# Performance work log

Hardware: AMD Instinct MI355X
Metric: run time of the kernel (lower is better)

## Reference

```python
import jax, jax.numpy as jnp
from jax import lax
import numpy as np

FEAT_SIZES = [38, 19, 10, 5, 3, 1]
IN_CH = [512, 1024, 512, 256, 256, 256]
NUM_ANCH = [4, 6, 6, 6, 4, 4]
NUM_CLASSES = 91
BATCH = 32


def _conv3x3(x, w, b):
    # x: [N, C, H, W], w: [O, C, 3, 3] (OIHW), padding=1, stride=1
    y = lax.conv_general_dilated(x, w, window_strides=(1, 1), padding=((1, 1), (1, 1)),
                                 dimension_numbers=("NCHW", "OIHW", "NCHW"))
    return y + b[None, :, None, None]


def _scoring_head(feats, ws, bs, num_cols):
    # Faithful to SSDScoringHead.forward: per-level conv, reshape
    # (N, A*num_cols, H, W) -> (N, H*W*A, num_cols), concat over levels.
    outs = []
    for x, w, b in zip(feats, ws, bs):
        r = _conv3x3(x, w, b)
        N, _, H, W = r.shape
        r = r.reshape(N, -1, num_cols, H, W)          # [N, A, C, H, W]
        r = jnp.transpose(r, (0, 3, 4, 1, 2))          # [N, H, W, A, C]
        r = r.reshape(N, -1, num_cols)                 # [N, H*W*A, C]
        outs.append(r)
    return jnp.concatenate(outs, axis=1)


def setup_inputs() -> dict:
    key = jax.random.key(0)
    inp = {}
    k = key
    for i, (c, s, a) in enumerate(zip(IN_CH, FEAT_SIZES, NUM_ANCH)):
        k, k1, k2, k3 = jax.random.split(k, 4)
        inp[f"feat{i}"] = jax.random.normal(k1, (BATCH, c, s, s), dtype=jnp.float32)
        fan = c * 9
        scale = (2.0 / fan) ** 0.5
        inp[f"cls_w{i}"] = jax.random.normal(k2, (NUM_CLASSES * a, c, 3, 3), dtype=jnp.float32) * scale
        inp[f"cls_b{i}"] = jnp.zeros((NUM_CLASSES * a,), dtype=jnp.float32)
        inp[f"reg_w{i}"] = jax.random.normal(k3, (4 * a, c, 3, 3), dtype=jnp.float32) * scale
        inp[f"reg_b{i}"] = jnp.zeros((4 * a,), dtype=jnp.float32)
    return inp


def reference(feat0, feat1, feat2, feat3, feat4, feat5,
              cls_w0, cls_b0, reg_w0, reg_b0,
              cls_w1, cls_b1, reg_w1, reg_b1,
              cls_w2, cls_b2, reg_w2, reg_b2,
              cls_w3, cls_b3, reg_w3, reg_b3,
              cls_w4, cls_b4, reg_w4, reg_b4,
              cls_w5, cls_b5, reg_w5, reg_b5):
    feats = [feat0, feat1, feat2, feat3, feat4, feat5]
    cls_ws = [cls_w0, cls_w1, cls_w2, cls_w3, cls_w4, cls_w5]
    cls_bs = [cls_b0, cls_b1, cls_b2, cls_b3, cls_b4, cls_b5]
    reg_ws = [reg_w0, reg_w1, reg_w2, reg_w3, reg_w4, reg_w5]
    reg_bs = [reg_b0, reg_b1, reg_b2, reg_b3, reg_b4, reg_b5]
    bbox_regression = _scoring_head(feats, reg_ws, reg_bs, 4)          # [N, 8732, 4]
    cls_logits = _scoring_head(feats, cls_ws, cls_bs, NUM_CLASSES)     # [N, 8732, 91]
    return (bbox_regression, cls_logits)
```

## Files before the change

kernel.cpp:

```cpp
#include <hip/hip_runtime.h>

typedef __attribute__((ext_vector_type(8))) short short8;
typedef __attribute__((ext_vector_type(4))) short short4x;
typedef __attribute__((ext_vector_type(4))) float floatx4;

#define DEVI __device__ __forceinline__

#define GLL(g, l) __builtin_amdgcn_global_load_lds(                      \
    (const __attribute__((address_space(1))) void*)(g),                  \
    (__attribute__((address_space(3))) void*)(l), 16, 0, 0)

constexpr int LC[6]   = {512, 1024, 512, 256, 256, 256};
constexpr int LS[6]   = {38, 19, 10, 5, 3, 1};
constexpr int LA[6]   = {4, 6, 6, 6, 4, 4};
constexpr int LROW[6] = {0, 5776, 7942, 8542, 8692, 8728};
constexpr long FOFF[6] = {0, 23658496, 35487744, 37126144, 37330944, 37404672};
constexpr long WCBASE  = 37412864;
constexpr long WOFF[6] = {0, 1751040, 7004160, 9630720, 10944000, 11819520};
constexpr long ZOFF    = 50107904;
constexpr int  ZSIZE   = 1088;
constexpr long CLSOFF  = 1117696;
constexpr size_t WS_NEEDED = (size_t)(ZOFF + ZSIZE) * 2;

constexpr int RSTART[7] = {0, 380, 950, 1520, 2090, 2470, 2850};
constexpr int GB_T5 = 0, GB_T4 = 8, GB_T3 = 16, GB_T2 = 40, GB_T1 = 112, GB_T0 = 344, GB_TOT = 888;

DEVI short f2bf(float f) {
    union { float f; unsigned u; } x; x.f = f;
    unsigned u = x.u + 0x7fffu + ((x.u >> 16) & 1u);
    return (short)(u >> 16);
}

template<int L>
__global__ void transpose_feat(const float* __restrict__ feat, short* __restrict__ ft) {
    constexpr int C = LC[L], S = LS[L], HW = S * S;
    const int n  = blockIdx.z;
    const int p0 = blockIdx.x * 64;
    const int c0 = blockIdx.y * 64;
    __shared__ float tile[64][65];
    const int t = threadIdx.x;
    const float* fb = feat + ((size_t)n * C + c0) * HW;
#pragma unroll
    for (int e = 0; e < 16; ++e) {
        int idx = e * 256 + t;
        int p = idx & 63, cc = idx >> 6;
        int pix = p0 + p;
        tile[cc][p] = (pix < HW) ? fb[(size_t)cc * HW + pix] : 0.f;
    }
    __syncthreads();
    short* ob = ft + ((size_t)n * HW) * C + c0;
#pragma unroll
    for (int e = 0; e < 16; ++e) {
        int idx = e * 256 + t;
        int cc = idx & 63, p = idx >> 6;
        int pix = p0 + p;
        if (pix < HW) ob[(size_t)pix * C + cc] = f2bf(tile[cc][p]);
    }
}

struct WPtrs { const float* cw[6]; const float* rw[6]; };

template<int L>
DEVI void reorder_body(int o, const float* cw, const float* rw, short* wc, short* wlds) {
    constexpr int C = LC[L], K9 = 9 * C, A4 = 4 * LA[L];
    constexpr int LC2 = (C == 1024) ? 10 : (C == 512 ? 9 : 8);
    const int tid = threadIdx.x;
    const float* src = (o < A4) ? rw + (size_t)o * K9 : cw + (size_t)(o - A4) * K9;
#pragma unroll 1
    for (int i4 = tid; i4 < K9 / 4; i4 += 256) {
        floatx4 v = *(const floatx4*)(src + 4 * i4);
        short4x s;
#pragma unroll
        for (int j = 0; j < 4; ++j) s[j] = f2bf(v[j]);
        *(short4x*)(wlds + 4 * i4) = s;
    }
    __syncthreads();
    short* dst = wc + WOFF[L] + (size_t)o * K9;
#pragma unroll 1
    for (int g = tid; g < K9 / 8; g += 256) {
        const int k0 = g * 8;
        const int r  = k0 >> LC2;
        const int c0 = k0 & (C - 1);
        short8 v;
#pragma unroll
        for (int j = 0; j < 8; ++j) v[j] = wlds[(c0 + j) * 9 + r];
        *(short8*)(dst + k0) = v;
    }
}

__global__ __launch_bounds__(256)
void reorder_weights2(WPtrs p, short* __restrict__ wc, short* __restrict__ zb) {
    __shared__ short wlds[9216];
    const int b = blockIdx.x;
    if (b >= RSTART[6]) {
        if (threadIdx.x < ZSIZE / 8) {
            short8 z;
#pragma unroll
            for (int q = 0; q < 8; ++q) z[q] = 0;
            *(short8*)(zb + threadIdx.x * 8) = z;
        }
        return;
    }
    if (b >= RSTART[5])      reorder_body<5>(b - RSTART[5], p.cw[5], p.rw[5], wc, wlds);
    else if (b >= RSTART[4]) reorder_body<4>(b - RSTART[4], p.cw[4], p.rw[4], wc, wlds);
    else if (b >= RSTART[3]) reorder_body<3>(b - RSTART[3], p.cw[3], p.rw[3], wc, wlds);
    else if (b >= RSTART[2]) reorder_body<2>(b - RSTART[2], p.cw[2], p.rw[2], wc, wlds);
    else if (b >= RSTART[1]) reorder_body<1>(b - RSTART[1], p.cw[1], p.rw[1], wc, wlds);
    else                     reorder_body<0>(b,             p.cw[0], p.rw[0], wc, wlds);
}

template<int L>
DEVI void gemm_body(int lb, short* As, short* Bs,
                    const short* ft, const short* wc, const short* zb,
                    const float* cls_b, const float* reg_b, float* out)
{
    constexpr int C = LC[L], S = LS[L], A = LA[L];
    constexpr int HW = S * S, M = 32 * HW, K = 9 * C, O = 95 * A;
    constexpr int ROWOFF = LROW[L], A4 = 4 * A;
    constexpr int NM = (M + 255) / 256, NB = (O + 127) / 128;
    constexpr int TOT = NM * NB, TPX = (TOT + 7) / 8;
    constexpr int KC  = C / 32;
    constexpr int LKC = (C == 1024) ? 5 : (C == 512 ? 4 : 3);
    constexpr int NK  = 9 * KC;

    const int tt = (lb & 7) * TPX + (lb >> 3);
    if (tt >= TOT) return;
    const int m0 = (tt / NB) * 256;
    const int n0 = (tt % NB) * 128;

    const int t    = threadIdx.x;
    const int lane = t & 63;
    const int wid  = t >> 6;
    const int lrow = lane >> 2;
    const int kqe  = (lane & 3) ^ ((lane >> 3) & 3);

    const short* abase[4]; unsigned vmask[4];
#pragma unroll
    for (int j = 0; j < 4; ++j) {
        int m = m0 + wid * 64 + j * 16 + lrow;
        int mm = m < M ? m : (M - 1);
        int n = mm / HW;
        int rem = mm - n * HW;
        int y = rem / S, x = rem - (rem / S) * S;
        abase[j] = ft + ((size_t)n * HW + rem) * C + kqe * 8;
        unsigned msk = 0;
#pragma unroll
        for (int r = 0; r < 9; ++r) {
            int dy = r / 3 - 1, dx = r % 3 - 1;
            if ((unsigned)(y + dy) < (unsigned)S && (unsigned)(x + dx) < (unsigned)S)
                msk |= 1u << r;
        }
        vmask[j] = msk;
    }
    const short* bbase[2];
#pragma unroll
    for (int j = 0; j < 2; ++j) {
        int o = n0 + wid * 32 + j * 16 + lrow;
        if (o >= O) o = O - 1;
        bbase[j] = wc + (size_t)o * K + kqe * 8;
    }
    const short* zbl = zb + kqe * 8;

    const int wm    = (wid & 1) * 128;
    const int wn    = (wid >> 1) * 64;
    const int lcol  = lane & 15;
    const int lquad = lane >> 4;
    const int rq8   = (lquad ^ ((lcol >> 1) & 3)) * 8;

    floatx4 acc[8][4];
#pragma unroll
    for (int i = 0; i < 8; ++i)
#pragma unroll
        for (int j = 0; j < 4; ++j)
#pragma unroll
            for (int q = 0; q < 4; ++q) acc[i][j][q] = 0.f;

    auto stage = [&](int kk, int p) {
        const int r  = kk >> LKC;
        const int c0 = (kk & (KC - 1)) << 5;
        const int dy = r / 3 - 1, dx = r - (r / 3) * 3 - 1;
        const int roA = (dy * S + dx) * C + c0;
        const int roB = r * C + c0;
        short* ap = As + p * 8192;
        short* bp = Bs + p * 4096;
#pragma unroll
        for (int j = 0; j < 4; ++j) {
            const short* pa = ((vmask[j] >> r) & 1) ? abase[j] + roA : zbl + c0;
            GLL(pa, ap + (wid * 64 + j * 16) * 32);
        }
        GLL(bbase[0] + roB, bp + (wid * 32) * 32);
        GLL(bbase[1] + roB, bp + (wid * 32 + 16) * 32);
    };
    auto frags = [&](int p, short8* af, short8* bfr) {
        const short* ap = As + p * 8192;
        const short* bp = Bs + p * 4096;
#pragma unroll
        for (int f = 0; f < 8; ++f)
            af[f] = *(const short8*)&ap[(wm + f * 16 + lcol) * 32 + rq8];
#pragma unroll
        for (int f = 0; f < 4; ++f)
            bfr[f] = *(const short8*)&bp[(wn + f * 16 + lcol) * 32 + rq8];
    };
    auto mmac = [&](short8* af, short8* bfr) {
#pragma unroll
        for (int i = 0; i < 8; ++i)
#pragma unroll
            for (int j = 0; j < 4; ++j)
                acc[i][j] = __builtin_amdgcn_mfma_f32_16x16x32_bf16(af[i], bfr[j], acc[i][j], 0, 0, 0);
    };

    stage(0, 0);
    stage(1, 1);
    asm volatile("s_waitcnt vmcnt(6)" ::: "memory");
    __builtin_amdgcn_s_barrier();
    int p = 0, pn = 2;
#pragma unroll 1
    for (int kk = 0; kk < NK - 2; ++kk) {
        short8 af[8], bfr[4];
        frags(p, af, bfr);
        stage(kk + 2, pn);
        asm volatile("s_waitcnt vmcnt(6)" ::: "memory");
        __builtin_amdgcn_s_barrier();
        asm volatile("s_waitcnt lgkmcnt(0)" ::: "memory");
        __builtin_amdgcn_s_setprio(1);
        mmac(af, bfr);
        __builtin_amdgcn_s_setprio(0);
        __builtin_amdgcn_s_barrier();
        p  = (p  == 2) ? 0 : p  + 1;
        pn = (pn == 2) ? 0 : pn + 1;
    }
    {
        short8 af[8], bfr[4];
        frags((NK - 2) % 3, af, bfr);
        asm volatile("s_waitcnt vmcnt(0)" ::: "memory");
        __builtin_amdgcn_s_barrier();
        asm volatile("s_waitcnt lgkmcnt(0)" ::: "memory");
        __builtin_amdgcn_s_setprio(1);
        mmac(af, bfr);
        __builtin_amdgcn_s_setprio(0);
    }
    {
        short8 af[8], bfr[4];
        frags((NK - 1) % 3, af, bfr);
        mmac(af, bfr);
    }

    float* const bbox = out;
    float* const cls  = out + CLSOFF;
#pragma unroll
    for (int fn = 0; fn < 4; ++fn) {
        const int o = n0 + wn + fn * 16 + lcol;
        if (o < O) {
            if (o < A4) {
                const int aa = o >> 2, cc = o & 3;
                const float bias = reg_b[o];
#pragma unroll
                for (int fm = 0; fm < 8; ++fm)
#pragma unroll
                    for (int rg = 0; rg < 4; ++rg) {
                        int mr = m0 + wm + fm * 16 + lquad * 4 + rg;
                        if (mr < M) {
                            int n = mr / HW, rem = mr - n * HW;
                            bbox[((size_t)n * 8732 + ROWOFF + rem * A + aa) * 4 + cc] = acc[fm][fn][rg] + bias;
                        }
                    }
            } else {
                const int oc = o - A4;
                const int aa = oc / 91, cc = oc - aa * 91;
                const float bias = cls_b[oc];
#pragma unroll
                for (int fm = 0; fm < 8; ++fm)
#pragma unroll
                    for (int rg = 0; rg < 4; ++rg) {
                        int mr = m0 + wm + fm * 16 + lquad * 4 + rg;
                        if (mr < M) {
                            int n = mr / HW, rem = mr - n * HW;
                            cls[((size_t)n * 8732 + ROWOFF + rem * A + aa) * 91 + cc] = acc[fm][fn][rg] + bias;
                        }
                    }
            }
        }
    }
}

struct GArgs {
    const short* ft[6];
    const short* wcL[6];
    const short* zb;
    const float* cb[6];
    const float* rb[6];
    float* out;
};

__global__ __launch_bounds__(256, 2)
void gemm_all(GArgs a) {
    __shared__ __align__(16) short As[3 * 8192];
    __shared__ __align__(16) short Bs[3 * 4096];
    const int b = blockIdx.x;
    if (b >= GB_T0)      gemm_body<0>(b - GB_T0, As, Bs, a.ft[0], a.wcL[0], a.zb, a.cb[0], a.rb[0], a.out);
    else if (b >= GB_T1) gemm_body<1>(b - GB_T1, As, Bs, a.ft[1], a.wcL[1], a.zb, a.cb[1], a.rb[1], a.out);
    else if (b >= GB_T2) gemm_body<2>(b - GB_T2, As, Bs, a.ft[2], a.wcL[2], a.zb, a.cb[2], a.rb[2], a.out);
    else if (b >= GB_T3) gemm_body<3>(b - GB_T3, As, Bs, a.ft[3], a.wcL[3], a.zb, a.cb[3], a.rb[3], a.out);
    else if (b >= GB_T4) gemm_body<4>(b - GB_T4, As, Bs, a.ft[4], a.wcL[4], a.zb, a.cb[4], a.rb[4], a.out);
    else                 gemm_body<5>(b - GB_T5, As, Bs, a.ft[5], a.wcL[5], a.zb, a.cb[5], a.rb[5], a.out);
}

template<int L>
__global__ void naive_conv(const float* __restrict__ feat,
                           const float* __restrict__ cw, const float* __restrict__ cb,
                           const float* __restrict__ rw, const float* __restrict__ rb,
                           float* __restrict__ out)
{
    constexpr int C = LC[L], S = LS[L], A = LA[L];
    constexpr int HW = S * S, M = 32 * HW, A4 = 4 * A, ROWOFF = LROW[L];
    int m = blockIdx.x * 256 + threadIdx.x;
    if (m >= M) return;
    int o = blockIdx.y;
    int n = m / HW, rem = m - n * HW, h = rem / S, w = rem - (rem / S) * S;
    bool isreg = o < A4;
    const float* wr = isreg ? (rw + (size_t)o * C * 9) : (cw + (size_t)(o - A4) * C * 9);
    float sum = isreg ? rb[o] : cb[o - A4];
    const float* fb = feat + (size_t)n * C * HW;
    for (int c = 0; c < C; ++c) {
#pragma unroll
        for (int r = 0; r < 9; ++r) {
            int y = h + r / 3 - 1, x = w + r % 3 - 1;
            if ((unsigned)y < (unsigned)S && (unsigned)x < (unsigned)S)
                sum += wr[c * 9 + r] * fb[(size_t)c * HW + y * S + x];
        }
    }
    int rowidx = ROWOFF + rem * A;
    if (isreg) out[((size_t)n * 8732 + rowidx + (o >> 2)) * 4 + (o & 3)] = sum;
    else {
        int oc = o - A4;
        int a = oc / 91;
        (out + CLSOFF)[((size_t)n * 8732 + rowidx + a) * 91 + (oc - a * 91)] = sum;
    }
}

extern "C" void kernel_launch(void* const* d_in, const int* in_sizes, int n_in,
                              void* d_out, int out_size, void* d_ws, size_t ws_size,
                              hipStream_t stream)
{
    const float *feat[6], *cw[6], *cb[6], *rw[6], *rb[6];
    for (int i = 0; i < 6; ++i) {
        feat[i] = (const float*)d_in[5 * i + 0];
        cw[i]   = (const float*)d_in[5 * i + 1];
        cb[i]   = (const float*)d_in[5 * i + 2];
        rw[i]   = (const float*)d_in[5 * i + 3];
        rb[i]   = (const float*)d_in[5 * i + 4];
    }
    float* out = (float*)d_out;

    if (ws_size >= WS_NEEDED) {
        short* ws  = (short*)d_ws;
        short* wcp = ws + WCBASE;
        short* zb  = ws + ZOFF;
        transpose_feat<0><<<dim3(23, 8, 32), 256, 0, stream>>>(feat[0], ws + FOFF[0]);
        transpose_feat<1><<<dim3(6, 16, 32), 256, 0, stream>>>(feat[1], ws + FOFF[1]);
        transpose_feat<2><<<dim3(2, 8, 32), 256, 0, stream>>>(feat[2], ws + FOFF[2]);
        transpose_feat<3><<<dim3(1, 4, 32), 256, 0, stream>>>(feat[3], ws + FOFF[3]);
        transpose_feat<4><<<dim3(1, 4, 32), 256, 0, stream>>>(feat[4], ws + FOFF[4]);
        transpose_feat<5><<<dim3(1, 4, 32), 256, 0, stream>>>(feat[5], ws + FOFF[5]);
        WPtrs wp;
        for (int i = 0; i < 6; ++i) { wp.cw[i] = cw[i]; wp.rw[i] = rw[i]; }
        reorder_weights2<<<RSTART[6] + 1, 256, 0, stream>>>(wp, wcp, zb);
        GArgs ga;
        for (int i = 0; i < 6; ++i) {
            ga.ft[i]  = ws + FOFF[i];
            ga.wcL[i] = wcp + WOFF[i];
            ga.cb[i]  = cb[i];
            ga.rb[i]  = rb[i];
        }
        ga.zb  = zb;
        ga.out = out;
        gemm_all<<<GB_TOT, 256, 0, stream>>>(ga);
    } else {
        naive_conv<0><<<dim3(181, 380), 256, 0, stream>>>(feat[0], cw[0], cb[0], rw[0], rb[0], out);
        naive_conv<1><<<dim3(46, 570),  256, 0, stream>>>(feat[1], cw[1], cb[1], rw[1], rb[1], out);
        naive_conv<2><<<dim3(13, 570),  256, 0, stream>>>(feat[2], cw[2], cb[2], rw[2], rb[2], out);
        naive_conv<3><<<dim3(4, 570),   256, 0, stream>>>(feat[3], cw[3], cb[3], rw[3], rb[3], out);
        naive_conv<4><<<dim3(2, 380),   256, 0, stream>>>(feat[4], cw[4], cb[4], rw[4], rb[4], out);
        naive_conv<5><<<dim3(1, 380),   256, 0, stream>>>(feat[5], cw[5], cb[5], rw[5], rb[5], out);
    }
}
```

Baseline: 715.1 us.

## Merge prep kernels into one launch and restructure GEMM k-loop barrier pipeline

Folds the six feature transpose kernels, the weight reorder kernel and the zero-fill into a single prep_all launch that dispatches on block index over a shared LDS buffer, removing several launches and the tail gaps between them. The GEMM main loop now issues the next stage's global-to-LDS loads before reading fragments, uses a sched_barrier, and defers the vmcnt wait and barrier until after the MFMAs, leaving one barrier per iteration instead of two. This is meant to overlap LDS fragment reads and global loads with matrix math. With the triple buffer, the correctness of the single barrier depends on the buffer rotation keeping stage and read slots apart.

```diff
diff --git a/kernel.cpp b/kernel.cpp
--- a/kernel.cpp
+++ b/kernel.cpp
@@ -25,6 +25,13 @@
 constexpr int RSTART[7] = {0, 380, 950, 1520, 2090, 2470, 2850};
 constexpr int GB_T5 = 0, GB_T4 = 8, GB_T3 = 16, GB_T2 = 40, GB_T1 = 112, GB_T0 = 344, GB_TOT = 888;
 
+constexpr int PPX[6] = {23, 6, 2, 1, 1, 1};
+constexpr int PCY[6] = {8, 16, 8, 4, 4, 4};
+constexpr int PSTART[7] = {0, 5888, 8960, 9472, 9600, 9728, 9856};
+constexpr int PREORD = 9856;
+constexpr int PZERO  = PREORD + 2850;
+constexpr int PTOT   = PZERO + 1;
+
 DEVI short f2bf(float f) {
     union { float f; unsigned u; } x; x.f = f;
     unsigned u = x.u + 0x7fffu + ((x.u >> 16) & 1u);
@@ -32,12 +39,11 @@
 }
 
 template<int L>
-__global__ void transpose_feat(const float* __restrict__ feat, short* __restrict__ ft) {
+DEVI void transpose_body(int bx, int by, int n, const float* __restrict__ feat,
+                         short* __restrict__ ft, float (*tile)[65]) {
     constexpr int C = LC[L], S = LS[L], HW = S * S;
-    const int n  = blockIdx.z;
-    const int p0 = blockIdx.x * 64;
-    const int c0 = blockIdx.y * 64;
-    __shared__ float tile[64][65];
+    const int p0 = bx * 64;
+    const int c0 = by * 64;
     const int t = threadIdx.x;
     const float* fb = feat + ((size_t)n * C + c0) * HW;
 #pragma unroll
@@ -57,8 +63,6 @@
         if (pix < HW) ob[(size_t)pix * C + cc] = f2bf(tile[cc][p]);
     }
 }
-
-struct WPtrs { const float* cw[6]; const float* rw[6]; };
 
 template<int L>
 DEVI void reorder_body(int o, const float* cw, const float* rw, short* wc, short* wlds) {
@@ -88,25 +92,56 @@
     }
 }
 
+struct PrepArgs {
+    const float* feat[6];
+    const float* cw[6];
+    const float* rw[6];
+    short* ft[6];
+    short* wc;
+    short* zb;
+};
+
 __global__ __launch_bounds__(256)
-void reorder_weights2(WPtrs p, short* __restrict__ wc, short* __restrict__ zb) {
-    __shared__ short wlds[9216];
+void prep_all(PrepArgs a) {
+    __shared__ __align__(16) char PL[18432];
+    float (*tile)[65] = reinterpret_cast<float(*)[65]>(PL);
+    short* wlds = reinterpret_cast<short*>(PL);
     const int b = blockIdx.x;
-    if (b >= RSTART[6]) {
+    if (b >= PZERO) {
         if (threadIdx.x < ZSIZE / 8) {
             short8 z;
 #pragma unroll
             for (int q = 0; q < 8; ++q) z[q] = 0;
-            *(short8*)(zb + threadIdx.x * 8) = z;
+            *(short8*)(a.zb + threadIdx.x * 8) = z;
         }
         return;
     }
-    if (b >= RSTART[5])      reorder_body<5>(b - RSTART[5], p.cw[5], p.rw[5], wc, wlds);
-    else if (b >= RSTART[4]) reorder_body<4>(b - RSTART[4], p.cw[4], p.rw[4], wc, wlds);
-    else if (b >= RSTART[3]) reorder_body<3>(b - RSTART[3], p.cw[3], p.rw[3], wc, wlds);
-    else if (b >= RSTART[2]) reorder_body<2>(b - RSTART[2], p.cw[2], p.rw[2], wc, wlds);
-    else if (b >= RSTART[1]) reorder_body<1>(b - RSTART[1], p.cw[1], p.rw[1], wc, wlds);
-    else                     reorder_body<0>(b,             p.cw[0], p.rw[0], wc, wlds);
+    if (b >= PREORD) {
+        int rb = b - PREORD;
+        if (rb >= RSTART[5])      reorder_body<5>(rb - RSTART[5], a.cw[5], a.rw[5], a.wc, wlds);
+        else if (rb >= RSTART[4]) reorder_body<4>(rb - RSTART[4], a.cw[4], a.rw[4], a.wc, wlds);
+        else if (rb >= RSTART[3]) reorder_body<3>(rb - RSTART[3], a.cw[3], a.rw[3], a.wc, wlds);
+        else if (rb >= RSTART[2]) reorder_body<2>(rb - RSTART[2], a.cw[2], a.rw[2], a.wc, wlds);
+        else if (rb >= RSTART[1]) reorder_body<1>(rb - RSTART[1], a.cw[1], a.rw[1], a.wc, wlds);
+        else                      reorder_body<0>(rb,             a.cw[0], a.rw[0], a.wc, wlds);
+        return;
+    }
+#define TDISP(L)                                                              \
+    {                                                                         \
+        int r = b - PSTART[L];                                                \
+        int bx = r % PPX[L];                                                  \
+        int by = (r / PPX[L]) % PCY[L];                                       \
+        int n  = r / (PPX[L] * PCY[L]);                                       \
+        transpose_body<L>(bx, by, n, a.feat[L], a.ft[L], tile);               \
+        return;                                                               \
+    }
+    if (b >= PSTART[5])      TDISP(5)
+    else if (b >= PSTART[4]) TDISP(4)
+    else if (b >= PSTART[3]) TDISP(3)
+    else if (b >= PSTART[2]) TDISP(2)
+    else if (b >= PSTART[1]) TDISP(1)
+    else                     TDISP(0)
+#undef TDISP
 }
 
 template<int L>
@@ -217,31 +252,30 @@
 #pragma unroll 1
     for (int kk = 0; kk < NK - 2; ++kk) {
         short8 af[8], bfr[4];
+        stage(kk + 2, pn);
         frags(p, af, bfr);
-        stage(kk + 2, pn);
-        asm volatile("s_waitcnt vmcnt(6)" ::: "memory");
-        __builtin_amdgcn_s_barrier();
-        asm volatile("s_waitcnt lgkmcnt(0)" ::: "memory");
+        __builtin_amdgcn_sched_barrier(0);
         __builtin_amdgcn_s_setprio(1);
         mmac(af, bfr);
         __builtin_amdgcn_s_setprio(0);
+        asm volatile("s_waitcnt vmcnt(6)" ::: "memory");
         __builtin_amdgcn_s_barrier();
         p  = (p  == 2) ? 0 : p  + 1;
         pn = (pn == 2) ? 0 : pn + 1;
     }
     {
         short8 af[8], bfr[4];
-        frags((NK - 2) % 3, af, bfr);
-        asm volatile("s_waitcnt vmcnt(0)" ::: "memory");
-        __builtin_amdgcn_s_barrier();
-        asm volatile("s_waitcnt lgkmcnt(0)" ::: "memory");
+        frags(p, af, bfr);
         __builtin_amdgcn_s_setprio(1);
         mmac(af, bfr);
         __builtin_amdgcn_s_setprio(0);
+        asm volatile("s_waitcnt vmcnt(0)" ::: "memory");
+        __builtin_amdgcn_s_barrier();
+        p = (p == 2) ? 0 : p + 1;
     }
     {
         short8 af[8], bfr[4];
-        frags((NK - 1) % 3, af, bfr);
+        frags(p, af, bfr);
         mmac(af, bfr);
     }
 
@@ -356,15 +390,16 @@
         short* ws  = (short*)d_ws;
         short* wcp = ws + WCBASE;
         short* zb  = ws + ZOFF;
-        transpose_feat<0><<<dim3(23, 8, 32), 256, 0, stream>>>(feat[0], ws + FOFF[0]);
-        transpose_feat<1><<<dim3(6, 16, 32), 256, 0, stream>>>(feat[1], ws + FOFF[1]);
-        transpose_feat<2><<<dim3(2, 8, 32), 256, 0, stream>>>(feat[2], ws + FOFF[2]);
-        transpose_feat<3><<<dim3(1, 4, 32), 256, 0, stream>>>(feat[3], ws + FOFF[3]);
-        transpose_feat<4><<<dim3(1, 4, 32), 256, 0, stream>>>(feat[4], ws + FOFF[4]);
-        transpose_feat<5><<<dim3(1, 4, 32), 256, 0, stream>>>(feat[5], ws + FOFF[5]);
-        WPtrs wp;
-        for (int i = 0; i < 6; ++i) { wp.cw[i] = cw[i]; wp.rw[i] = rw[i]; }
-        reorder_weights2<<<RSTART[6] + 1, 256, 0, stream>>>(wp, wcp, zb);
+        PrepArgs pa;
+        for (int i = 0; i < 6; ++i) {
+            pa.feat[i] = feat[i];
+            pa.cw[i]   = cw[i];
+            pa.rw[i]   = rw[i];
+            pa.ft[i]   = ws + FOFF[i];
+        }
+        pa.wc = wcp;
+        pa.zb = zb;
+        prep_all<<<PTOT, 256, 0, stream>>>(pa);
         GArgs ga;
         for (int i = 0; i < 6; ++i) {
             ga.ft[i]  = ws + FOFF[i];
```

Result: slower. 744.1 us (+4.0%).
